# Optimization experiments

Hardware: AMD Instinct MI355X
Metric: run time of the kernel (lower is better)

Reference implementation:

```python
import jax, jax.numpy as jnp
import numpy as np

SEQ, BATCH, IN, HID, OUT = 512, 64, 512, 1024, 512
KEEP = 0.7  # dropout p = 0.3


def setup_inputs() -> dict:
    key = jax.random.key(0)
    ks = jax.random.split(key, 9)
    def lin(k, fan_out, fan_in):
        bound = 1.0 / np.sqrt(fan_in)
        kw, kb = jax.random.split(k)
        W = jax.random.uniform(kw, (fan_out, fan_in), jnp.float32, -bound, bound)
        b = jax.random.uniform(kb, (fan_out,), jnp.float32, -bound, bound)
        return W, b
    x = jax.random.normal(ks[0], (SEQ, BATCH, IN), jnp.float32)
    # inverted dropout mask, fixed for determinism
    drop_mask = (jax.random.bernoulli(ks[1], KEEP, (SEQ, BATCH, OUT))
                 .astype(jnp.float32) / KEEP)
    W_i2h, b_i2h = lin(ks[2], HID, IN + HID)
    W_i2o, b_i2o = lin(ks[3], OUT, IN + HID)
    W_o2o, b_o2o = lin(ks[4], OUT, HID + OUT)
    return {"x": x, "drop_mask": drop_mask,
            "W_i2h": W_i2h, "b_i2h": b_i2h,
            "W_i2o": W_i2o, "b_i2o": b_i2o,
            "W_o2o": W_o2o, "b_o2o": b_o2o}


def reference(x, drop_mask, W_i2h, b_i2h, W_i2o, b_i2o, W_o2o, b_o2o):
    # x: [S, B, IN]; returns log-probs [S, B, OUT]
    def step(h, inp):
        x_t, m_t = inp  # [B, IN], [B, OUT]
        comb = jnp.concatenate([x_t, h], axis=1)          # [B, IN+HID]
        out = comb @ W_i2o.T + b_i2o                      # [B, OUT]
        h_new = comb @ W_i2h.T + b_i2h                    # [B, HID]
        oc = jnp.concatenate([out, h_new], axis=1) @ W_o2o.T + b_o2o  # [B, OUT]
        oc = oc * m_t                                     # dropout (inverted mask)
        oc = jax.nn.log_softmax(oc, axis=-1)
        return h_new, oc
    h0 = jnp.zeros((x.shape[1], W_i2h.shape[0]), x.dtype)
    _, outs = jax.lax.scan(step, h0, (x, drop_mask))
    return outs
```

## Files before the change

kernel.cpp:

```cpp
#include <hip/hip_runtime.h>
#include <stdint.h>


typedef unsigned short ushort_t;
typedef __attribute__((ext_vector_type(8))) __bf16 bf16x8;
typedef __attribute__((ext_vector_type(4))) float f32x4;

__device__ __forceinline__ ushort_t f2bf(float f) {
  union { float f; uint32_t u; } v; v.f = f;
  uint32_t r = v.u + 0x7fffu + ((v.u >> 16) & 1u);
  return (ushort_t)(r >> 16);
}
__device__ __forceinline__ float bf2f(ushort_t b) {
  union { uint32_t u; float f; } v; v.u = ((uint32_t)b) << 16;
  return v.f;
}

__device__ __forceinline__ void gload16(const ushort_t* g, ushort_t* l) {
  __builtin_amdgcn_global_load_lds(
      (const __attribute__((address_space(1))) uint32_t*)g,
      (__attribute__((address_space(3))) uint32_t*)l, 16, 0, 0);
}

__global__ __launch_bounds__(256) void init_kernel(uint32_t* harr0) {
  int i = blockIdx.x * blockDim.x + threadIdx.x;
  if (i < 32768) harr0[i] = 0;
}

__global__ __launch_bounds__(256) void pack_kernel(
    const float* __restrict__ x, const float* __restrict__ W_i2h,
    const float* __restrict__ W_i2o, const float* __restrict__ W_o2o,
    ushort_t* xB, ushort_t* Wihx, ushort_t* Whh, ushort_t* Wiox,
    ushort_t* Wioh, ushort_t* Wo1, ushort_t* Wo2) {
  int64_t i = (int64_t)blockIdx.x * blockDim.x + threadIdx.x;
  const int64_t c0 = 16777216, c1 = 17301504, c2 = 18350080, c3 = 18612224,
                c4 = 19136512, c5 = 19398656, c6 = 19922944;
  if (i < c0) { xB[i] = f2bf(x[i]); return; }
  if (i < c1) { int64_t j = i - c0; int r = j >> 9,  c = j & 511;  Wihx[j] = f2bf(W_i2h[(int64_t)r * 1536 + c]); return; }
  if (i < c2) { int64_t j = i - c1; int r = j >> 10, c = j & 1023; Whh[j]  = f2bf(W_i2h[(int64_t)r * 1536 + 512 + c]); return; }
  if (i < c3) { int64_t j = i - c2; int r = j >> 9,  c = j & 511;  Wiox[j] = f2bf(W_i2o[(int64_t)r * 1536 + c]); return; }
  if (i < c4) { int64_t j = i - c3; int r = j >> 10, c = j & 1023; Wioh[j] = f2bf(W_i2o[(int64_t)r * 1536 + 512 + c]); return; }
  if (i < c5) { int64_t j = i - c4; int r = j >> 9,  c = j & 511;  Wo1[j]  = f2bf(W_o2o[(int64_t)r * 1536 + c]); return; }
  if (i < c6) { int64_t j = i - c5; int r = j >> 10, c = j & 1023; Wo2[j]  = f2bf(W_o2o[(int64_t)r * 1536 + 512 + c]); return; }
}

__global__ __launch_bounds__(256) void gemm_bt(
    const ushort_t* __restrict__ A1, int lda1, const ushort_t* __restrict__ B1, int K1,
    const ushort_t* __restrict__ A2, int lda2, const ushort_t* __restrict__ B2, int K2,
    const float* __restrict__ bias, float* Cf, ushort_t* Cb, int Ntiles) {
  __shared__ __align__(16) ushort_t AsF[4096];
  __shared__ __align__(16) ushort_t BsF[4096];
  const int mt = blockIdx.x & 255, nt = blockIdx.x >> 8;
  const int m0 = mt * 128, n0 = nt * 128;
  const int tid = threadIdx.x;
  const int w = tid >> 6, l = tid & 63;
  const int quad = l >> 4, l15 = l & 15;
  const int wm = (w & 1) * 64, wn = (w >> 1) * 64;
  const int r0 = tid >> 2, chunk = tid & 3;
  f32x4 acc[4][4] = {};

  for (int phase = 0; phase < 2; ++phase) {
    const ushort_t* A = phase ? A2 : A1;
    const ushort_t* B = phase ? B2 : B1;
    const int lda = phase ? lda2 : lda1;
    const int K = phase ? K2 : K1;
    for (int k0 = 0; k0 < K; k0 += 32) {
      __syncthreads();
      gload16(A + (size_t)(m0 + r0) * lda + k0 + chunk * 8,      &AsF[tid * 8]);
      gload16(A + (size_t)(m0 + r0 + 64) * lda + k0 + chunk * 8, &AsF[2048 + tid * 8]);
      gload16(B + (size_t)(n0 + r0) * K + k0 + chunk * 8,        &BsF[tid * 8]);
      gload16(B + (size_t)(n0 + r0 + 64) * K + k0 + chunk * 8,   &BsF[2048 + tid * 8]);
      __syncthreads();
      bf16x8 af[4], bfr[4];
#pragma unroll
      for (int i = 0; i < 4; ++i) af[i]  = *(const bf16x8*)&AsF[(wm + 16 * i + l15) * 32 + 8 * quad];
#pragma unroll
      for (int j = 0; j < 4; ++j) bfr[j] = *(const bf16x8*)&BsF[(wn + 16 * j + l15) * 32 + 8 * quad];
#pragma unroll
      for (int i = 0; i < 4; ++i)
#pragma unroll
        for (int j = 0; j < 4; ++j)
          acc[i][j] = __builtin_amdgcn_mfma_f32_16x16x32_bf16(af[i], bfr[j], acc[i][j], 0, 0, 0);
    }
  }

  const int N = Ntiles * 128;
#pragma unroll
  for (int i = 0; i < 4; ++i) {
    const int row = m0 + wm + 16 * i + 4 * quad;
#pragma unroll
    for (int j = 0; j < 4; ++j) {
      const int col = n0 + wn + 16 * j + l15;
      const float bv = bias[col];
#pragma unroll
      for (int r = 0; r < 4; ++r) {
        const float v = acc[i][j][r] + bv;
        const size_t idx = (size_t)(row + r) * N + col;
        if (Cf) Cf[idx] = v;
        else Cb[idx] = f2bf(v);
      }
    }
  }
}

__global__ __launch_bounds__(256) void gemm_bn(
    const ushort_t* __restrict__ Am, const ushort_t* __restrict__ Bm,
    ushort_t* __restrict__ Om) {
  __shared__ __align__(16) ushort_t AsF[4096];
  __shared__ __align__(16) ushort_t BsF[4096];
  const int mt = blockIdx.x >> 3, nt = blockIdx.x & 7;
  const int m0 = mt * 128, n0 = nt * 128;
  const int tid = threadIdx.x;
  const int w = tid >> 6, l = tid & 63;
  const int quad = l >> 4, l15 = l & 15;
  const int wm = (w & 1) * 64, wn = (w >> 1) * 64;
  const int r0 = tid >> 2, chunk = tid & 3;
  f32x4 acc[4][4] = {};
  for (int k0 = 0; k0 < 1024; k0 += 32) {
    __syncthreads();
    gload16(Am + (size_t)(m0 + r0) * 1024 + k0 + chunk * 8,      &AsF[tid * 8]);
    gload16(Am + (size_t)(m0 + r0 + 64) * 1024 + k0 + chunk * 8, &AsF[2048 + tid * 8]);
#pragma unroll
    for (int rep = 0; rep < 2; ++rep) {
      const int idx = tid + 256 * rep;
      const int kk = idx & 31, n8 = idx >> 5;
      union { uint4 v; ushort_t s[8]; } u;
      u.v = *(const uint4*)(Bm + (size_t)(k0 + kk) * 1024 + n0 + n8 * 8);
#pragma unroll
      for (int i = 0; i < 8; ++i) BsF[(n8 * 8 + i) * 32 + kk] = u.s[i];
    }
    __syncthreads();
    bf16x8 af[4], bfr[4];
#pragma unroll
    for (int i = 0; i < 4; ++i) af[i]  = *(const bf16x8*)&AsF[(wm + 16 * i + l15) * 32 + 8 * quad];
#pragma unroll
    for (int j = 0; j < 4; ++j) bfr[j] = *(const bf16x8*)&BsF[(wn + 16 * j + l15) * 32 + 8 * quad];
#pragma unroll
    for (int i = 0; i < 4; ++i)
#pragma unroll
      for (int j = 0; j < 4; ++j)
        acc[i][j] = __builtin_amdgcn_mfma_f32_16x16x32_bf16(af[i], bfr[j], acc[i][j], 0, 0, 0);
  }
#pragma unroll
  for (int i = 0; i < 4; ++i) {
    const int row = m0 + wm + 16 * i + 4 * quad;
#pragma unroll
    for (int j = 0; j < 4; ++j) {
      const int col = n0 + wn + 16 * j + l15;
#pragma unroll
      for (int r = 0; r < 4; ++r)
        Om[(size_t)(row + r) * 1024 + col] = f2bf(acc[i][j][r]);
    }
  }
}

__global__ __launch_bounds__(256) void rnn_step(
    const ushort_t* __restrict__ A, size_t aStride,
    const ushort_t* __restrict__ Xh, const ushort_t* __restrict__ Whh,
    ushort_t* __restrict__ O) {
  __shared__ __align__(16) ushort_t AsF[4096];
  __shared__ __align__(16) ushort_t BsF[4096];
  const int p = blockIdx.x >> 3;
  const int n0 = (blockIdx.x & 7) * 128;
  const int tid = threadIdx.x;
  const int w = tid >> 6, l = tid & 63;
  const int quad = l >> 4, l15 = l & 15;
  const int wm = (w & 1) * 64, wn = (w >> 1) * 64;
  const int r0 = tid >> 2, chunk = tid & 3;
  f32x4 acc[4][4] = {};
  const ushort_t* a0 = A + (size_t)(2 * p) * aStride + (size_t)r0 * 1024;
  const ushort_t* a1 = A + (size_t)(2 * p + 1) * aStride + (size_t)r0 * 1024;
  for (int k0 = 0; k0 < 1024; k0 += 32) {
    __syncthreads();
    gload16(a0 + k0 + chunk * 8, &AsF[tid * 8]);
    gload16(a1 + k0 + chunk * 8, &AsF[2048 + tid * 8]);
    gload16(Whh + (size_t)(n0 + r0) * 1024 + k0 + chunk * 8,      &BsF[tid * 8]);
    gload16(Whh + (size_t)(n0 + r0 + 64) * 1024 + k0 + chunk * 8, &BsF[2048 + tid * 8]);
    __syncthreads();
    bf16x8 af[4], bfr[4];
#pragma unroll
    for (int i = 0; i < 4; ++i) af[i]  = *(const bf16x8*)&AsF[(wm + 16 * i + l15) * 32 + 8 * quad];
#pragma unroll
    for (int j = 0; j < 4; ++j) bfr[j] = *(const bf16x8*)&BsF[(wn + 16 * j + l15) * 32 + 8 * quad];
#pragma unroll
    for (int i = 0; i < 4; ++i)
#pragma unroll
      for (int j = 0; j < 4; ++j)
        acc[i][j] = __builtin_amdgcn_mfma_f32_16x16x32_bf16(af[i], bfr[j], acc[i][j], 0, 0, 0);
  }
#pragma unroll
  for (int i = 0; i < 4; ++i) {
#pragma unroll
    for (int j = 0; j < 4; ++j) {
      const int col = n0 + wn + 16 * j + l15;
#pragma unroll
      for (int r = 0; r < 4; ++r) {
        const int gr = wm + 16 * i + 4 * quad + r;
        const int c = 2 * p + (gr >> 6);
        const size_t idx = (size_t)c * 524288 + (size_t)(gr & 63) * 1024 + col;
        O[idx] = f2bf(acc[i][j][r] + bf2f(Xh[idx]));
      }
    }
  }
}

__global__ __launch_bounds__(256) void scan_step(
    const ushort_t* __restrict__ Sold, const ushort_t* __restrict__ V,
    ushort_t* __restrict__ Snew, int d) {
  __shared__ __align__(16) ushort_t AsF[4096];
  __shared__ __align__(16) ushort_t BsF[4096];
  const int p = blockIdx.x >> 3;
  const int n0 = (blockIdx.x & 7) * 128;
  const int tid = threadIdx.x;
  const int w = tid >> 6, l = tid & 63;
  const int quad = l >> 4, l15 = l & 15;
  const int wm = (w & 1) * 64, wn = (w >> 1) * 64;
  const int r0 = tid >> 2, chunk = tid & 3;
  f32x4 acc[4][4] = {};
  const int j0 = 2 * p, j1 = 2 * p + 1;
  const int s0 = (j0 >= d) ? j0 - d : j0;
  const int s1 = (j1 >= d) ? j1 - d : j1;
  const ushort_t* a0 = Sold + (size_t)s0 * 65536 + (size_t)r0 * 1024;
  const ushort_t* a1 = Sold + (size_t)s1 * 65536 + (size_t)r0 * 1024;
  for (int k0 = 0; k0 < 1024; k0 += 32) {
    __syncthreads();
    gload16(a0 + k0 + chunk * 8, &AsF[tid * 8]);
    gload16(a1 + k0 + chunk * 8, &AsF[2048 + tid * 8]);
    gload16(V + (size_t)(n0 + r0) * 1024 + k0 + chunk * 8,      &BsF[tid * 8]);
    gload16(V + (size_t)(n0 + r0 + 64) * 1024 + k0 + chunk * 8, &BsF[2048 + tid * 8]);
    __syncthreads();
    bf16x8 af[4], bfr[4];
#pragma unroll
    for (int i = 0; i < 4; ++i) af[i]  = *(const bf16x8*)&AsF[(wm + 16 * i + l15) * 32 + 8 * quad];
#pragma unroll
    for (int j = 0; j < 4; ++j) bfr[j] = *(const bf16x8*)&BsF[(wn + 16 * j + l15) * 32 + 8 * quad];
#pragma unroll
    for (int i = 0; i < 4; ++i)
#pragma unroll
      for (int j = 0; j < 4; ++j)
        acc[i][j] = __builtin_amdgcn_mfma_f32_16x16x32_bf16(af[i], bfr[j], acc[i][j], 0, 0, 0);
  }
#pragma unroll
  for (int i = 0; i < 4; ++i) {
#pragma unroll
    for (int j = 0; j < 4; ++j) {
      const int col = n0 + wn + 16 * j + l15;
#pragma unroll
      for (int r = 0; r < 4; ++r) {
        const int gr = wm + 16 * i + 4 * quad + r;
        const int c = 2 * p + (gr >> 6);
        const size_t idx = (size_t)c * 65536 + (size_t)(gr & 63) * 1024 + col;
        const float g = (c >= d) ? acc[i][j][r] : 0.0f;
        Snew[idx] = f2bf(g + bf2f(Sold[idx]));
      }
    }
  }
}

__global__ __launch_bounds__(256) void correct_kernel(
    const ushort_t* __restrict__ S, ushort_t* __restrict__ Harr,
    const ushort_t* __restrict__ B1, const ushort_t* __restrict__ B2,
    const ushort_t* __restrict__ B3, const ushort_t* __restrict__ B4,
    const ushort_t* __restrict__ B5, const ushort_t* __restrict__ B6,
    const ushort_t* __restrict__ B7, const ushort_t* __restrict__ B8) {
  __shared__ __align__(16) ushort_t AsF[4096];
  __shared__ __align__(16) ushort_t BsF[4096];
  const int p = blockIdx.x >> 3;
  const int n0 = (blockIdx.x & 7) * 128;
  const int j = blockIdx.y + 1;
  const ushort_t* Wj;
  switch (j) {
    case 1: Wj = B1; break; case 2: Wj = B2; break;
    case 3: Wj = B3; break; case 4: Wj = B4; break;
    case 5: Wj = B5; break; case 6: Wj = B6; break;
    case 7: Wj = B7; break; default: Wj = B8; break;
  }
  ushort_t* XO = Harr + (size_t)j * 65536;
  const int tid = threadIdx.x;
  const int w = tid >> 6, l = tid & 63;
  const int quad = l >> 4, l15 = l & 15;
  const int wm = (w & 1) * 64, wn = (w >> 1) * 64;
  const int r0 = tid >> 2, chunk = tid & 3;
  f32x4 acc[4][4] = {};
  const ushort_t* a0 = S + (size_t)(2 * p) * 65536 + (size_t)r0 * 1024;
  const ushort_t* a1 = S + (size_t)(2 * p + 1) * 65536 + (size_t)r0 * 1024;
  for (int k0 = 0; k0 < 1024; k0 += 32) {
    __syncthreads();
    gload16(a0 + k0 + chunk * 8, &AsF[tid * 8]);
    gload16(a1 + k0 + chunk * 8, &AsF[2048 + tid * 8]);
    gload16(Wj + (size_t)(n0 + r0) * 1024 + k0 + chunk * 8,      &BsF[tid * 8]);
    gload16(Wj + (size_t)(n0 + r0 + 64) * 1024 + k0 + chunk * 8, &BsF[2048 + tid * 8]);
    __syncthreads();
    bf16x8 af[4], bfr[4];
#pragma unroll
    for (int i = 0; i < 4; ++i) af[i]  = *(const bf16x8*)&AsF[(wm + 16 * i + l15) * 32 + 8 * quad];
#pragma unroll
    for (int jj = 0; jj < 4; ++jj) bfr[jj] = *(const bf16x8*)&BsF[(wn + 16 * jj + l15) * 32 + 8 * quad];
#pragma unroll
    for (int i = 0; i < 4; ++i)
#pragma unroll
      for (int jj = 0; jj < 4; ++jj)
        acc[i][jj] = __builtin_amdgcn_mfma_f32_16x16x32_bf16(af[i], bfr[jj], acc[i][jj], 0, 0, 0);
  }
#pragma unroll
  for (int i = 0; i < 4; ++i) {
#pragma unroll
    for (int jj = 0; jj < 4; ++jj) {
      const int col = n0 + wn + 16 * jj + l15;
#pragma unroll
      for (int r = 0; r < 4; ++r) {
        const int gr = wm + 16 * i + 4 * quad + r;
        const int c = 2 * p + (gr >> 6);
        const size_t idx = (size_t)c * 524288 + (size_t)(gr & 63) * 1024 + col;
        XO[idx] = f2bf(acc[i][jj][r] + bf2f(XO[idx]));
      }
    }
  }
}

__global__ __launch_bounds__(256) void copy_strided(
    ushort_t* __restrict__ dst, size_t dStride,
    const ushort_t* __restrict__ src, size_t sStride) {
  const int c = blockIdx.x >> 5, part = blockIdx.x & 31;
  const size_t off = (size_t)part * 2048 + (size_t)threadIdx.x * 8;
  *(uint4*)(dst + (size_t)c * dStride + off) = *(const uint4*)(src + (size_t)c * sStride + off);
}

__global__ __launch_bounds__(256) void softmax_kernel(
    float* __restrict__ out, const float* __restrict__ mask) {
  const int row = blockIdx.x;
  const int tid = threadIdx.x;
  const size_t base = (size_t)row * 512;
  __shared__ float sm[4], ss[4];
  const float v0 = out[base + tid] * mask[base + tid];
  const float v1 = out[base + tid + 256] * mask[base + tid + 256];
  float m = fmaxf(v0, v1);
#pragma unroll
  for (int off = 32; off; off >>= 1) m = fmaxf(m, __shfl_xor(m, off, 64));
  const int w = tid >> 6;
  if ((tid & 63) == 0) sm[w] = m;
  __syncthreads();
  m = fmaxf(fmaxf(sm[0], sm[1]), fmaxf(sm[2], sm[3]));
  float s = __expf(v0 - m) + __expf(v1 - m);
#pragma unroll
  for (int off = 32; off; off >>= 1) s += __shfl_xor(s, off, 64);
  if ((tid & 63) == 0) ss[w] = s;
  __syncthreads();
  s = ss[0] + ss[1] + ss[2] + ss[3];
  const float lg = logf(s);
  out[base + tid] = v0 - m - lg;
  out[base + tid + 256] = v1 - m - lg;
}

extern "C" void kernel_launch(void* const* d_in, const int* in_sizes, int n_in,
                              void* d_out, int out_size, void* d_ws, size_t ws_size,
                              hipStream_t stream) {
  const float* x     = (const float*)d_in[0];
  const float* mask  = (const float*)d_in[1];
  const float* W_i2h = (const float*)d_in[2];
  const float* b_i2h = (const float*)d_in[3];
  const float* W_i2o = (const float*)d_in[4];
  const float* b_i2o = (const float*)d_in[5];
  const float* W_o2o = (const float*)d_in[6];
  const float* b_o2o = (const float*)d_in[7];
  float* out = (float*)d_out;

  char* ws = (char*)d_ws;
  const size_t NEED = 207753216;
  if (ws_size < NEED) return;
  ushort_t* xB   = (ushort_t*)(ws + 0);
  ushort_t* XhB  = (ushort_t*)(ws + 33554432);
  ushort_t* Harr = (ushort_t*)(ws + 100663296);
  char* outbRegion = ws + 167903232;
  ushort_t* OUTB = (ushort_t*)outbRegion;
  ushort_t* SA = (ushort_t*)(outbRegion + 0);
  ushort_t* SB = (ushort_t*)(outbRegion + 8388608);
  ushort_t* PB = (ushort_t*)(outbRegion + 16777216);
  ushort_t* P2 = PB, *P4 = PB + 1048576, *P8 = PB + 2097152,
          * S3 = PB + 3145728, *S5 = PB + 4194304, *S6 = PB + 5242880,
          * S7 = PB + 6291456, *P256 = PB + 7340032;
  ushort_t* P16 = S3, *P32 = S5, *P64 = S6, *P128 = S7;
  ushort_t* Wihx = (ushort_t*)(ws + 201457664);
  ushort_t* Whh  = (ushort_t*)(ws + 202506240);
  ushort_t* Wiox = (ushort_t*)(ws + 204603392);
  ushort_t* Wioh = (ushort_t*)(ws + 205127680);
  ushort_t* Wo1  = (ushort_t*)(ws + 206176256);
  ushort_t* Wo2  = (ushort_t*)(ws + 206700544);

  hipLaunchKernelGGL(init_kernel, dim3(128), dim3(256), 0, stream, (uint32_t*)Harr);
  hipLaunchKernelGGL(pack_kernel, dim3(77824), dim3(256), 0, stream,
                     x, W_i2h, W_i2o, W_o2o, xB, Wihx, Whh, Wiox, Wioh, Wo1, Wo2);
  hipLaunchKernelGGL(gemm_bt, dim3(2048), dim3(256), 0, stream,
                     xB, 512, Wihx, 512, (const ushort_t*)nullptr, 0,
                     (const ushort_t*)nullptr, 0, b_i2h, (float*)nullptr, XhB, 8);
  hipLaunchKernelGGL(gemm_bn, dim3(64), dim3(256), 0, stream, Whh, Whh, P2);
  hipLaunchKernelGGL(gemm_bn, dim3(64), dim3(256), 0, stream, P2, P2, P4);
  hipLaunchKernelGGL(gemm_bn, dim3(64), dim3(256), 0, stream, P4, P4, P8);
  hipLaunchKernelGGL(gemm_bn, dim3(64), dim3(256), 0, stream, P8, P8, P16);
  hipLaunchKernelGGL(gemm_bn, dim3(64), dim3(256), 0, stream, P16, P16, P32);
  hipLaunchKernelGGL(gemm_bn, dim3(64), dim3(256), 0, stream, P32, P32, P64);
  hipLaunchKernelGGL(gemm_bn, dim3(64), dim3(256), 0, stream, P64, P64, P128);
  hipLaunchKernelGGL(gemm_bn, dim3(64), dim3(256), 0, stream, P128, P128, P256);
  hipLaunchKernelGGL(copy_strided, dim3(2048), dim3(256), 0, stream,
                     Harr + 65536, (size_t)524288, XhB, (size_t)524288);
  for (int k = 1; k < 8; ++k)
    hipLaunchKernelGGL(rnn_step, dim3(256), dim3(256), 0, stream,
                       Harr + (size_t)k * 65536, (size_t)524288,
                       XhB + (size_t)k * 65536, Whh, Harr + (size_t)(k + 1) * 65536);
  hipLaunchKernelGGL(copy_strided, dim3(2048), dim3(256), 0, stream,
                     SA, (size_t)65536, Harr, (size_t)524288);
  hipLaunchKernelGGL(scan_step, dim3(256), dim3(256), 0, stream, SA, P8,   SB, 1);
  hipLaunchKernelGGL(scan_step, dim3(256), dim3(256), 0, stream, SB, P16,  SA, 2);
  hipLaunchKernelGGL(scan_step, dim3(256), dim3(256), 0, stream, SA, P32,  SB, 4);
  hipLaunchKernelGGL(scan_step, dim3(256), dim3(256), 0, stream, SB, P64,  SA, 8);
  hipLaunchKernelGGL(scan_step, dim3(256), dim3(256), 0, stream, SA, P128, SB, 16);
  hipLaunchKernelGGL(scan_step, dim3(256), dim3(256), 0, stream, SB, P256, SA, 32);
  hipLaunchKernelGGL(gemm_bn, dim3(64), dim3(256), 0, stream, Whh, P2, S3);
  hipLaunchKernelGGL(gemm_bn, dim3(64), dim3(256), 0, stream, Whh, P4, S5);
  hipLaunchKernelGGL(gemm_bn, dim3(64), dim3(256), 0, stream, P2,  P4, S6);
  hipLaunchKernelGGL(gemm_bn, dim3(64), dim3(256), 0, stream, S3,  P4, S7);
  hipLaunchKernelGGL(correct_kernel, dim3(256, 8), dim3(256), 0, stream,
                     SA, Harr, Whh, P2, S3, P4, S5, S6, S7, P8);
  hipLaunchKernelGGL(gemm_bt, dim3(1024), dim3(256), 0, stream,
                     xB, 512, Wiox, 512, Harr, 1024, Wioh, 1024,
                     b_i2o, (float*)nullptr, OUTB, 4);
  hipLaunchKernelGGL(gemm_bt, dim3(1024), dim3(256), 0, stream,
                     OUTB, 512, Wo1, 512, Harr + 65536, 1024, Wo2, 1024,
                     b_o2o, out, (ushort_t*)nullptr, 4);
  hipLaunchKernelGGL(softmax_kernel, dim3(32768), dim3(256), 0, stream, out, mask);
}
```

Before: 1.254 ms.

## Fuse scan phases into persistent kernel and fold output projections algebraically

Replaces the many separate rnn_step, scan_step and power-matrix gemm launches with one persistent kernel of 256 blocks that uses a global atomic-counter barrier between stages. It also overlaps the power-matrix products with the recurrent steps. The output path is re-associated algebraically: W_o2o's first half is premultiplied into W_i2o (U1, U2) and a combined bias, so one fused GEMM with three K phases produces the logits directly, and the mask multiply moves into its epilogue. This removes launch overhead and the intermediate OUTB round trip. The costs are spin-wait grid barriers that assume all 256 blocks are co-resident, and a different bf16 rounding order in the folded weights.

```diff
diff --git a/kernel.cpp b/kernel.cpp
--- a/kernel.cpp
+++ b/kernel.cpp
@@ -15,26 +15,27 @@
   union { uint32_t u; float f; } v; v.u = ((uint32_t)b) << 16;
   return v.f;
 }
-
 __device__ __forceinline__ void gload16(const ushort_t* g, ushort_t* l) {
   __builtin_amdgcn_global_load_lds(
       (const __attribute__((address_space(1))) uint32_t*)g,
       (__attribute__((address_space(3))) uint32_t*)l, 16, 0, 0);
 }
 
-__global__ __launch_bounds__(256) void init_kernel(uint32_t* harr0) {
+__global__ __launch_bounds__(256) void init_kernel(uint32_t* harr0, int* cnt) {
   int i = blockIdx.x * blockDim.x + threadIdx.x;
   if (i < 32768) harr0[i] = 0;
+  if (i < 16) cnt[i] = 0;
 }
 
 __global__ __launch_bounds__(256) void pack_kernel(
     const float* __restrict__ x, const float* __restrict__ W_i2h,
     const float* __restrict__ W_i2o, const float* __restrict__ W_o2o,
+    const float* __restrict__ b_i2o, const float* __restrict__ b_o2o,
     ushort_t* xB, ushort_t* Wihx, ushort_t* Whh, ushort_t* Wiox,
-    ushort_t* Wioh, ushort_t* Wo1, ushort_t* Wo2) {
+    ushort_t* Wioh, ushort_t* Wo1, ushort_t* Wo2, float* biasP) {
   int64_t i = (int64_t)blockIdx.x * blockDim.x + threadIdx.x;
   const int64_t c0 = 16777216, c1 = 17301504, c2 = 18350080, c3 = 18612224,
-                c4 = 19136512, c5 = 19398656, c6 = 19922944;
+                c4 = 19136512, c5 = 19398656, c6 = 19922944, c7 = 19923456;
   if (i < c0) { xB[i] = f2bf(x[i]); return; }
   if (i < c1) { int64_t j = i - c0; int r = j >> 9,  c = j & 511;  Wihx[j] = f2bf(W_i2h[(int64_t)r * 1536 + c]); return; }
   if (i < c2) { int64_t j = i - c1; int r = j >> 10, c = j & 1023; Whh[j]  = f2bf(W_i2h[(int64_t)r * 1536 + 512 + c]); return; }
@@ -42,12 +43,18 @@
   if (i < c4) { int64_t j = i - c3; int r = j >> 10, c = j & 1023; Wioh[j] = f2bf(W_i2o[(int64_t)r * 1536 + 512 + c]); return; }
   if (i < c5) { int64_t j = i - c4; int r = j >> 9,  c = j & 511;  Wo1[j]  = f2bf(W_o2o[(int64_t)r * 1536 + c]); return; }
   if (i < c6) { int64_t j = i - c5; int r = j >> 10, c = j & 1023; Wo2[j]  = f2bf(W_o2o[(int64_t)r * 1536 + 512 + c]); return; }
+  if (i < c7) {
+    int n = (int)(i - c6);
+    const float* wr = W_o2o + (int64_t)n * 1536;
+    float s = 0.f;
+    for (int m = 0; m < 512; ++m) s += wr[m] * b_i2o[m];
+    biasP[n] = s + b_o2o[n];
+  }
 }
 
 __global__ __launch_bounds__(256) void gemm_bt(
     const ushort_t* __restrict__ A1, int lda1, const ushort_t* __restrict__ B1, int K1,
-    const ushort_t* __restrict__ A2, int lda2, const ushort_t* __restrict__ B2, int K2,
-    const float* __restrict__ bias, float* Cf, ushort_t* Cb, int Ntiles) {
+    const float* __restrict__ bias, ushort_t* Cb, int Ntiles) {
   __shared__ __align__(16) ushort_t AsF[4096];
   __shared__ __align__(16) ushort_t BsF[4096];
   const int mt = blockIdx.x & 255, nt = blockIdx.x >> 8;
@@ -58,32 +65,24 @@
   const int wm = (w & 1) * 64, wn = (w >> 1) * 64;
   const int r0 = tid >> 2, chunk = tid & 3;
   f32x4 acc[4][4] = {};
-
-  for (int phase = 0; phase < 2; ++phase) {
-    const ushort_t* A = phase ? A2 : A1;
-    const ushort_t* B = phase ? B2 : B1;
-    const int lda = phase ? lda2 : lda1;
-    const int K = phase ? K2 : K1;
-    for (int k0 = 0; k0 < K; k0 += 32) {
-      __syncthreads();
-      gload16(A + (size_t)(m0 + r0) * lda + k0 + chunk * 8,      &AsF[tid * 8]);
-      gload16(A + (size_t)(m0 + r0 + 64) * lda + k0 + chunk * 8, &AsF[2048 + tid * 8]);
-      gload16(B + (size_t)(n0 + r0) * K + k0 + chunk * 8,        &BsF[tid * 8]);
-      gload16(B + (size_t)(n0 + r0 + 64) * K + k0 + chunk * 8,   &BsF[2048 + tid * 8]);
-      __syncthreads();
-      bf16x8 af[4], bfr[4];
-#pragma unroll
-      for (int i = 0; i < 4; ++i) af[i]  = *(const bf16x8*)&AsF[(wm + 16 * i + l15) * 32 + 8 * quad];
-#pragma unroll
-      for (int j = 0; j < 4; ++j) bfr[j] = *(const bf16x8*)&BsF[(wn + 16 * j + l15) * 32 + 8 * quad];
-#pragma unroll
-      for (int i = 0; i < 4; ++i)
-#pragma unroll
-        for (int j = 0; j < 4; ++j)
-          acc[i][j] = __builtin_amdgcn_mfma_f32_16x16x32_bf16(af[i], bfr[j], acc[i][j], 0, 0, 0);
-    }
-  }
-
+  for (int k0 = 0; k0 < K1; k0 += 32) {
+    __syncthreads();
+    gload16(A1 + (size_t)(m0 + r0) * lda1 + k0 + chunk * 8,      &AsF[tid * 8]);
+    gload16(A1 + (size_t)(m0 + r0 + 64) * lda1 + k0 + chunk * 8, &AsF[2048 + tid * 8]);
+    gload16(B1 + (size_t)(n0 + r0) * K1 + k0 + chunk * 8,        &BsF[tid * 8]);
+    gload16(B1 + (size_t)(n0 + r0 + 64) * K1 + k0 + chunk * 8,   &BsF[2048 + tid * 8]);
+    __syncthreads();
+    bf16x8 af[4], bfr[4];
+#pragma unroll
+    for (int i = 0; i < 4; ++i) af[i]  = *(const bf16x8*)&AsF[(wm + 16 * i + l15) * 32 + 8 * quad];
+#pragma unroll
+    for (int j = 0; j < 4; ++j) bfr[j] = *(const bf16x8*)&BsF[(wn + 16 * j + l15) * 32 + 8 * quad];
+#pragma unroll
+    for (int i = 0; i < 4; ++i)
+#pragma unroll
+      for (int j = 0; j < 4; ++j)
+        acc[i][j] = __builtin_amdgcn_mfma_f32_16x16x32_bf16(af[i], bfr[j], acc[i][j], 0, 0, 0);
+  }
   const int N = Ntiles * 128;
 #pragma unroll
   for (int i = 0; i < 4; ++i) {
@@ -93,23 +92,74 @@
       const int col = n0 + wn + 16 * j + l15;
       const float bv = bias[col];
 #pragma unroll
-      for (int r = 0; r < 4; ++r) {
-        const float v = acc[i][j][r] + bv;
-        const size_t idx = (size_t)(row + r) * N + col;
-        if (Cf) Cf[idx] = v;
-        else Cb[idx] = f2bf(v);
-      }
-    }
-  }
-}
-
-__global__ __launch_bounds__(256) void gemm_bn(
-    const ushort_t* __restrict__ Am, const ushort_t* __restrict__ Bm,
-    ushort_t* __restrict__ Om) {
+      for (int r = 0; r < 4; ++r)
+        Cb[(size_t)(row + r) * N + col] = f2bf(acc[i][j][r] + bv);
+    }
+  }
+}
+
+__global__ __launch_bounds__(256) void usetup_kernel(
+    const ushort_t* __restrict__ Wo1, const ushort_t* __restrict__ Wiox,
+    const ushort_t* __restrict__ Wioh, ushort_t* __restrict__ U1,
+    ushort_t* __restrict__ U2) {
   __shared__ __align__(16) ushort_t AsF[4096];
   __shared__ __align__(16) ushort_t BsF[4096];
-  const int mt = blockIdx.x >> 3, nt = blockIdx.x & 7;
+  int job = blockIdx.x;
+  const ushort_t* Bm; ushort_t* Om; int mt, nt, ldb;
+  if (job < 16) { mt = job >> 2; nt = job & 3; Bm = Wiox; Om = U1; ldb = 512; }
+  else { job -= 16; mt = job >> 3; nt = job & 7; Bm = Wioh; Om = U2; ldb = 1024; }
   const int m0 = mt * 128, n0 = nt * 128;
+  const int tid = threadIdx.x;
+  const int w = tid >> 6, l = tid & 63;
+  const int quad = l >> 4, l15 = l & 15;
+  const int wm = (w & 1) * 64, wn = (w >> 1) * 64;
+  const int r0 = tid >> 2, chunk = tid & 3;
+  f32x4 acc[4][4] = {};
+  for (int k0 = 0; k0 < 512; k0 += 32) {
+    __syncthreads();
+    gload16(Wo1 + (size_t)(m0 + r0) * 512 + k0 + chunk * 8,      &AsF[tid * 8]);
+    gload16(Wo1 + (size_t)(m0 + r0 + 64) * 512 + k0 + chunk * 8, &AsF[2048 + tid * 8]);
+#pragma unroll
+    for (int rep = 0; rep < 2; ++rep) {
+      const int idx = tid + 256 * rep;
+      const int kk = idx & 31, n8 = idx >> 5;
+      union { uint4 v; ushort_t s[8]; } u;
+      u.v = *(const uint4*)(Bm + (size_t)(k0 + kk) * ldb + n0 + n8 * 8);
+#pragma unroll
+      for (int i = 0; i < 8; ++i) BsF[(n8 * 8 + i) * 32 + kk] = u.s[i];
+    }
+    __syncthreads();
+    bf16x8 af[4], bfr[4];
+#pragma unroll
+    for (int i = 0; i < 4; ++i) af[i]  = *(const bf16x8*)&AsF[(wm + 16 * i + l15) * 32 + 8 * quad];
+#pragma unroll
+    for (int j = 0; j < 4; ++j) bfr[j] = *(const bf16x8*)&BsF[(wn + 16 * j + l15) * 32 + 8 * quad];
+#pragma unroll
+    for (int i = 0; i < 4; ++i)
+#pragma unroll
+      for (int j = 0; j < 4; ++j)
+        acc[i][j] = __builtin_amdgcn_mfma_f32_16x16x32_bf16(af[i], bfr[j], acc[i][j], 0, 0, 0);
+  }
+#pragma unroll
+  for (int i = 0; i < 4; ++i) {
+    const int row = m0 + wm + 16 * i + 4 * quad;
+#pragma unroll
+    for (int j = 0; j < 4; ++j) {
+      const int col = n0 + wn + 16 * j + l15;
+#pragma unroll
+      for (int r = 0; r < 4; ++r)
+        Om[(size_t)(row + r) * ldb + col] = f2bf(acc[i][j][r]);
+    }
+  }
+}
+
+__device__ void tile_job(
+    const ushort_t* a0, const ushort_t* a1,
+    const ushort_t* B, int btr, int n0,
+    const ushort_t* x0, const ushort_t* x1,
+    ushort_t* o0, ushort_t* o1, int g0, int g1) {
+  __shared__ __align__(16) ushort_t AsF[4096];
+  __shared__ __align__(16) ushort_t BsF[4096];
   const int tid = threadIdx.x;
   const int w = tid >> 6, l = tid & 63;
   const int quad = l >> 4, l15 = l & 15;
@@ -118,16 +168,21 @@
   f32x4 acc[4][4] = {};
   for (int k0 = 0; k0 < 1024; k0 += 32) {
     __syncthreads();
-    gload16(Am + (size_t)(m0 + r0) * 1024 + k0 + chunk * 8,      &AsF[tid * 8]);
-    gload16(Am + (size_t)(m0 + r0 + 64) * 1024 + k0 + chunk * 8, &AsF[2048 + tid * 8]);
-#pragma unroll
-    for (int rep = 0; rep < 2; ++rep) {
-      const int idx = tid + 256 * rep;
-      const int kk = idx & 31, n8 = idx >> 5;
-      union { uint4 v; ushort_t s[8]; } u;
-      u.v = *(const uint4*)(Bm + (size_t)(k0 + kk) * 1024 + n0 + n8 * 8);
-#pragma unroll
-      for (int i = 0; i < 8; ++i) BsF[(n8 * 8 + i) * 32 + kk] = u.s[i];
+    gload16(a0 + (size_t)r0 * 1024 + k0 + chunk * 8, &AsF[tid * 8]);
+    gload16(a1 + (size_t)r0 * 1024 + k0 + chunk * 8, &AsF[2048 + tid * 8]);
+    if (!btr) {
+      gload16(B + (size_t)(n0 + r0) * 1024 + k0 + chunk * 8,      &BsF[tid * 8]);
+      gload16(B + (size_t)(n0 + r0 + 64) * 1024 + k0 + chunk * 8, &BsF[2048 + tid * 8]);
+    } else {
+#pragma unroll
+      for (int rep = 0; rep < 2; ++rep) {
+        const int idx = tid + 256 * rep;
+        const int kk = idx & 31, n8 = idx >> 5;
+        union { uint4 v; ushort_t s[8]; } u;
+        u.v = *(const uint4*)(B + (size_t)(k0 + kk) * 1024 + n0 + n8 * 8);
+#pragma unroll
+        for (int i = 0; i < 8; ++i) BsF[(n8 * 8 + i) * 32 + kk] = u.s[i];
+      }
     }
     __syncthreads();
     bf16x8 af[4], bfr[4];
@@ -143,117 +198,106 @@
   }
 #pragma unroll
   for (int i = 0; i < 4; ++i) {
-    const int row = m0 + wm + 16 * i + 4 * quad;
 #pragma unroll
     for (int j = 0; j < 4; ++j) {
       const int col = n0 + wn + 16 * j + l15;
 #pragma unroll
-      for (int r = 0; r < 4; ++r)
-        Om[(size_t)(row + r) * 1024 + col] = f2bf(acc[i][j][r]);
-    }
-  }
-}
-
-__global__ __launch_bounds__(256) void rnn_step(
-    const ushort_t* __restrict__ A, size_t aStride,
-    const ushort_t* __restrict__ Xh, const ushort_t* __restrict__ Whh,
-    ushort_t* __restrict__ O) {
-  __shared__ __align__(16) ushort_t AsF[4096];
-  __shared__ __align__(16) ushort_t BsF[4096];
-  const int p = blockIdx.x >> 3;
-  const int n0 = (blockIdx.x & 7) * 128;
-  const int tid = threadIdx.x;
-  const int w = tid >> 6, l = tid & 63;
-  const int quad = l >> 4, l15 = l & 15;
-  const int wm = (w & 1) * 64, wn = (w >> 1) * 64;
-  const int r0 = tid >> 2, chunk = tid & 3;
-  f32x4 acc[4][4] = {};
-  const ushort_t* a0 = A + (size_t)(2 * p) * aStride + (size_t)r0 * 1024;
-  const ushort_t* a1 = A + (size_t)(2 * p + 1) * aStride + (size_t)r0 * 1024;
-  for (int k0 = 0; k0 < 1024; k0 += 32) {
-    __syncthreads();
-    gload16(a0 + k0 + chunk * 8, &AsF[tid * 8]);
-    gload16(a1 + k0 + chunk * 8, &AsF[2048 + tid * 8]);
-    gload16(Whh + (size_t)(n0 + r0) * 1024 + k0 + chunk * 8,      &BsF[tid * 8]);
-    gload16(Whh + (size_t)(n0 + r0 + 64) * 1024 + k0 + chunk * 8, &BsF[2048 + tid * 8]);
-    __syncthreads();
-    bf16x8 af[4], bfr[4];
-#pragma unroll
-    for (int i = 0; i < 4; ++i) af[i]  = *(const bf16x8*)&AsF[(wm + 16 * i + l15) * 32 + 8 * quad];
-#pragma unroll
-    for (int j = 0; j < 4; ++j) bfr[j] = *(const bf16x8*)&BsF[(wn + 16 * j + l15) * 32 + 8 * quad];
-#pragma unroll
-    for (int i = 0; i < 4; ++i)
-#pragma unroll
-      for (int j = 0; j < 4; ++j)
-        acc[i][j] = __builtin_amdgcn_mfma_f32_16x16x32_bf16(af[i], bfr[j], acc[i][j], 0, 0, 0);
-  }
-#pragma unroll
-  for (int i = 0; i < 4; ++i) {
-#pragma unroll
-    for (int j = 0; j < 4; ++j) {
-      const int col = n0 + wn + 16 * j + l15;
-#pragma unroll
       for (int r = 0; r < 4; ++r) {
         const int gr = wm + 16 * i + 4 * quad + r;
-        const int c = 2 * p + (gr >> 6);
-        const size_t idx = (size_t)c * 524288 + (size_t)(gr & 63) * 1024 + col;
-        O[idx] = f2bf(acc[i][j][r] + bf2f(Xh[idx]));
-      }
-    }
-  }
-}
-
-__global__ __launch_bounds__(256) void scan_step(
-    const ushort_t* __restrict__ Sold, const ushort_t* __restrict__ V,
-    ushort_t* __restrict__ Snew, int d) {
-  __shared__ __align__(16) ushort_t AsF[4096];
-  __shared__ __align__(16) ushort_t BsF[4096];
-  const int p = blockIdx.x >> 3;
-  const int n0 = (blockIdx.x & 7) * 128;
-  const int tid = threadIdx.x;
-  const int w = tid >> 6, l = tid & 63;
-  const int quad = l >> 4, l15 = l & 15;
-  const int wm = (w & 1) * 64, wn = (w >> 1) * 64;
-  const int r0 = tid >> 2, chunk = tid & 3;
-  f32x4 acc[4][4] = {};
-  const int j0 = 2 * p, j1 = 2 * p + 1;
-  const int s0 = (j0 >= d) ? j0 - d : j0;
-  const int s1 = (j1 >= d) ? j1 - d : j1;
-  const ushort_t* a0 = Sold + (size_t)s0 * 65536 + (size_t)r0 * 1024;
-  const ushort_t* a1 = Sold + (size_t)s1 * 65536 + (size_t)r0 * 1024;
-  for (int k0 = 0; k0 < 1024; k0 += 32) {
-    __syncthreads();
-    gload16(a0 + k0 + chunk * 8, &AsF[tid * 8]);
-    gload16(a1 + k0 + chunk * 8, &AsF[2048 + tid * 8]);
-    gload16(V + (size_t)(n0 + r0) * 1024 + k0 + chunk * 8,      &BsF[tid * 8]);
-    gload16(V + (size_t)(n0 + r0 + 64) * 1024 + k0 + chunk * 8, &BsF[2048 + tid * 8]);
-    __syncthreads();
-    bf16x8 af[4], bfr[4];
-#pragma unroll
-    for (int i = 0; i < 4; ++i) af[i]  = *(const bf16x8*)&AsF[(wm + 16 * i + l15) * 32 + 8 * quad];
-#pragma unroll
-    for (int j = 0; j < 4; ++j) bfr[j] = *(const bf16x8*)&BsF[(wn + 16 * j + l15) * 32 + 8 * quad];
-#pragma unroll
-    for (int i = 0; i < 4; ++i)
-#pragma unroll
-      for (int j = 0; j < 4; ++j)
-        acc[i][j] = __builtin_amdgcn_mfma_f32_16x16x32_bf16(af[i], bfr[j], acc[i][j], 0, 0, 0);
-  }
-#pragma unroll
-  for (int i = 0; i < 4; ++i) {
-#pragma unroll
-    for (int j = 0; j < 4; ++j) {
-      const int col = n0 + wn + 16 * j + l15;
-#pragma unroll
-      for (int r = 0; r < 4; ++r) {
-        const int gr = wm + 16 * i + 4 * quad + r;
-        const int c = 2 * p + (gr >> 6);
-        const size_t idx = (size_t)c * 65536 + (size_t)(gr & 63) * 1024 + col;
-        const float g = (c >= d) ? acc[i][j][r] : 0.0f;
-        Snew[idx] = f2bf(g + bf2f(Sold[idx]));
-      }
-    }
+        const int half = gr >> 6, rr = gr & 63;
+        float v = (half ? g1 : g0) ? acc[i][j][r] : 0.0f;
+        const ushort_t* xx = half ? x1 : x0;
+        if (xx) v += bf2f(xx[(size_t)rr * 1024 + col]);
+        (half ? o1 : o0)[(size_t)rr * 1024 + col] = f2bf(v);
+      }
+    }
+  }
+}
+
+__device__ __forceinline__ void gsync(int* cnt, int s) {
+  __threadfence();
+  __syncthreads();
+  if (threadIdx.x == 0) {
+    atomicAdd(&cnt[s], 1);
+    while (__hip_atomic_load(&cnt[s], __ATOMIC_RELAXED, __HIP_MEMORY_SCOPE_AGENT) < 256) {}
+  }
+  __syncthreads();
+  __threadfence();
+}
+
+#define PWp(idx) (Pw + (size_t)(idx) * 1048576)
+
+__global__ __launch_bounds__(256) void scan_mega(
+    const ushort_t* __restrict__ XhB, ushort_t* __restrict__ Harr,
+    ushort_t* __restrict__ Pw, ushort_t* __restrict__ SA,
+    ushort_t* __restrict__ SB, const ushort_t* __restrict__ Whh,
+    int* __restrict__ cnt) {
+  const int bid = blockIdx.x;
+  const int tid = threadIdx.x;
+
+  if (bid < 64) {
+    const ushort_t* src = XhB + (size_t)bid * 524288;
+    ushort_t* dst = Harr + 65536 + (size_t)bid * 524288;
+#pragma unroll
+    for (int it = 0; it < 32; ++it)
+      *(uint4*)(dst + it * 2048 + tid * 8) = *(const uint4*)(src + it * 2048 + tid * 8);
+  } else if (bid < 128) {
+    const int t = bid - 64, mt = t >> 3, nt = t & 7;
+    const ushort_t* a0 = Whh + (size_t)mt * 131072;
+    tile_job(a0, a0 + 65536, Whh, 1, nt * 128, nullptr, nullptr,
+             PWp(0) + (size_t)mt * 131072, PWp(0) + (size_t)mt * 131072 + 65536, 1, 1);
+  }
+  gsync(cnt, 0);
+
+  for (int k = 1; k <= 7; ++k) {
+    {
+      const int p = bid & 31, nt = bid >> 5;
+      const size_t c0 = (size_t)(2 * p) * 524288, c1 = c0 + 524288;
+      tile_job(Harr + (size_t)k * 65536 + c0, Harr + (size_t)k * 65536 + c1,
+               Whh, 0, nt * 128,
+               XhB + (size_t)k * 65536 + c0, XhB + (size_t)k * 65536 + c1,
+               Harr + (size_t)(k + 1) * 65536 + c0,
+               Harr + (size_t)(k + 1) * 65536 + c1, 1, 1);
+    }
+    {
+      const ushort_t *A = nullptr, *Bp = nullptr; ushort_t* O = nullptr;
+      const int pj = bid >> 6, t = bid & 63;
+      if (k == 1) {
+        if (pj == 0)      { A = Whh;    Bp = PWp(0); O = PWp(1); }
+        else if (pj == 1) { A = PWp(0); Bp = PWp(0); O = PWp(2); }
+      } else if (k == 2) {
+        if (pj == 0)      { A = Whh;    Bp = PWp(2); O = PWp(3); }
+        else if (pj == 1) { A = PWp(0); Bp = PWp(2); O = PWp(4); }
+        else if (pj == 2) { A = PWp(1); Bp = PWp(2); O = PWp(5); }
+        else              { A = PWp(2); Bp = PWp(2); O = PWp(6); }
+      } else if (pj == 0) {
+        A = PWp(3 + k); Bp = A; O = PWp(4 + k);
+      }
+      if (A) {
+        const int mt = t >> 3, nt2 = t & 7;
+        tile_job(A + (size_t)mt * 131072, A + (size_t)mt * 131072 + 65536,
+                 Bp, 1, nt2 * 128, nullptr, nullptr,
+                 O + (size_t)mt * 131072, O + (size_t)mt * 131072 + 65536, 1, 1);
+      }
+    }
+    gsync(cnt, k);
+  }
+
+  for (int si = 0; si < 6; ++si) {
+    const int d = 1 << si;
+    const ushort_t* oldB; size_t oldStr; ushort_t* nw;
+    if (si == 0)      { oldB = Harr; oldStr = 524288; nw = SB; }
+    else if (si & 1)  { oldB = SB;   oldStr = 65536;  nw = SA; }
+    else              { oldB = SA;   oldStr = 65536;  nw = SB; }
+    const int p = bid & 31, nt = bid >> 5;
+    const int ca = 2 * p, cb = ca + 1;
+    const int ia = ca >= d ? ca - d : ca, ib = cb >= d ? cb - d : cb;
+    tile_job(oldB + (size_t)ia * oldStr, oldB + (size_t)ib * oldStr,
+             PWp(6 + si), 0, nt * 128,
+             oldB + (size_t)ca * oldStr, oldB + (size_t)cb * oldStr,
+             nw + (size_t)ca * 65536, nw + (size_t)cb * 65536,
+             ca >= d, cb >= d);
+    if (si < 5) gsync(cnt, 8 + si);
   }
 }
 
@@ -318,22 +362,67 @@
   }
 }
 
-__global__ __launch_bounds__(256) void copy_strided(
-    ushort_t* __restrict__ dst, size_t dStride,
-    const ushort_t* __restrict__ src, size_t sStride) {
-  const int c = blockIdx.x >> 5, part = blockIdx.x & 31;
-  const size_t off = (size_t)part * 2048 + (size_t)threadIdx.x * 8;
-  *(uint4*)(dst + (size_t)c * dStride + off) = *(const uint4*)(src + (size_t)c * sStride + off);
-}
-
-__global__ __launch_bounds__(256) void softmax_kernel(
-    float* __restrict__ out, const float* __restrict__ mask) {
+__global__ __launch_bounds__(256) void gemm_fused(
+    const ushort_t* __restrict__ xB, const ushort_t* __restrict__ U1,
+    const ushort_t* __restrict__ Harr, const ushort_t* __restrict__ U2,
+    const ushort_t* __restrict__ Wo2, const float* __restrict__ biasP,
+    const float* __restrict__ mask, float* __restrict__ out) {
+  __shared__ __align__(16) ushort_t AsF[4096];
+  __shared__ __align__(16) ushort_t BsF[4096];
+  const int mt = blockIdx.x & 255, nt = blockIdx.x >> 8;
+  const int m0 = mt * 128, n0 = nt * 128;
+  const int tid = threadIdx.x;
+  const int w = tid >> 6, l = tid & 63;
+  const int quad = l >> 4, l15 = l & 15;
+  const int wm = (w & 1) * 64, wn = (w >> 1) * 64;
+  const int r0 = tid >> 2, chunk = tid & 3;
+  f32x4 acc[4][4] = {};
+  for (int ph = 0; ph < 3; ++ph) {
+    const ushort_t* A = ph == 0 ? xB : (ph == 1 ? Harr : Harr + 65536);
+    const ushort_t* B = ph == 0 ? U1 : (ph == 1 ? U2 : Wo2);
+    const int K = ph == 0 ? 512 : 1024;
+    for (int k0 = 0; k0 < K; k0 += 32) {
+      __syncthreads();
+      gload16(A + (size_t)(m0 + r0) * K + k0 + chunk * 8,      &AsF[tid * 8]);
+      gload16(A + (size_t)(m0 + r0 + 64) * K + k0 + chunk * 8, &AsF[2048 + tid * 8]);
+      gload16(B + (size_t)(n0 + r0) * K + k0 + chunk * 8,      &BsF[tid * 8]);
+      gload16(B + (size_t)(n0 + r0 + 64) * K + k0 + chunk * 8, &BsF[2048 + tid * 8]);
+      __syncthreads();
+      bf16x8 af[4], bfr[4];
+#pragma unroll
+      for (int i = 0; i < 4; ++i) af[i]  = *(const bf16x8*)&AsF[(wm + 16 * i + l15) * 32 + 8 * quad];
+#pragma unroll
+      for (int j = 0; j < 4; ++j) bfr[j] = *(const bf16x8*)&BsF[(wn + 16 * j + l15) * 32 + 8 * quad];
+#pragma unroll
+      for (int i = 0; i < 4; ++i)
+#pragma unroll
+        for (int j = 0; j < 4; ++j)
+          acc[i][j] = __builtin_amdgcn_mfma_f32_16x16x32_bf16(af[i], bfr[j], acc[i][j], 0, 0, 0);
+    }
+  }
+#pragma unroll
+  for (int i = 0; i < 4; ++i) {
+    const int row = m0 + wm + 16 * i + 4 * quad;
+#pragma unroll
+    for (int j = 0; j < 4; ++j) {
+      const int col = n0 + wn + 16 * j + l15;
+      const float bv = biasP[col];
+#pragma unroll
+      for (int r = 0; r < 4; ++r) {
+        const size_t idx = (size_t)(row + r) * 512 + col;
+        out[idx] = (acc[i][j][r] + bv) * mask[idx];
+      }
+    }
+  }
+}
+
+__global__ __launch_bounds__(256) void softmax_kernel(float* __restrict__ out) {
   const int row = blockIdx.x;
   const int tid = threadIdx.x;
   const size_t base = (size_t)row * 512;
   __shared__ float sm[4], ss[4];
-  const float v0 = out[base + tid] * mask[base + tid];
-  const float v1 = out[base + tid + 256] * mask[base + tid + 256];
+  const float v0 = out[base + tid];
+  const float v1 = out[base + tid + 256];
   float m = fmaxf(v0, v1);
 #pragma unroll
   for (int off = 32; off; off >>= 1) m = fmaxf(m, __shfl_xor(m, off, 64));
@@ -370,62 +459,37 @@
   if (ws_size < NEED) return;
   ushort_t* xB   = (ushort_t*)(ws + 0);
   ushort_t* XhB  = (ushort_t*)(ws + 33554432);
+  ushort_t* SA   = (ushort_t*)(ws + 33554432);
+  ushort_t* SB   = (ushort_t*)(ws + 41943040);
   ushort_t* Harr = (ushort_t*)(ws + 100663296);
-  char* outbRegion = ws + 167903232;
-  ushort_t* OUTB = (ushort_t*)outbRegion;
-  ushort_t* SA = (ushort_t*)(outbRegion + 0);
-  ushort_t* SB = (ushort_t*)(outbRegion + 8388608);
-  ushort_t* PB = (ushort_t*)(outbRegion + 16777216);
-  ushort_t* P2 = PB, *P4 = PB + 1048576, *P8 = PB + 2097152,
-          * S3 = PB + 3145728, *S5 = PB + 4194304, *S6 = PB + 5242880,
-          * S7 = PB + 6291456, *P256 = PB + 7340032;
-  ushort_t* P16 = S3, *P32 = S5, *P64 = S6, *P128 = S7;
+  ushort_t* Pw   = (ushort_t*)(ws + 167903232);
+  ushort_t* U1   = (ushort_t*)(ws + 193069056);
+  ushort_t* U2   = (ushort_t*)(ws + 193593344);
+  float* biasP   = (float*)(ws + 194641920);
   ushort_t* Wihx = (ushort_t*)(ws + 201457664);
   ushort_t* Whh  = (ushort_t*)(ws + 202506240);
   ushort_t* Wiox = (ushort_t*)(ws + 204603392);
   ushort_t* Wioh = (ushort_t*)(ws + 205127680);
   ushort_t* Wo1  = (ushort_t*)(ws + 206176256);
   ushort_t* Wo2  = (ushort_t*)(ws + 206700544);
-
-  hipLaunchKernelGGL(init_kernel, dim3(128), dim3(256), 0, stream, (uint32_t*)Harr);
-  hipLaunchKernelGGL(pack_kernel, dim3(77824), dim3(256), 0, stream,
-                     x, W_i2h, W_i2o, W_o2o, xB, Wihx, Whh, Wiox, Wioh, Wo1, Wo2);
+  int* cnt       = (int*)(ws + 207749120);
+
+  hipLaunchKernelGGL(init_kernel, dim3(128), dim3(256), 0, stream,
+                     (uint32_t*)Harr, cnt);
+  hipLaunchKernelGGL(pack_kernel, dim3(77826), dim3(256), 0, stream,
+                     x, W_i2h, W_i2o, W_o2o, b_i2o, b_o2o,
+                     xB, Wihx, Whh, Wiox, Wioh, Wo1, Wo2, biasP);
   hipLaunchKernelGGL(gemm_bt, dim3(2048), dim3(256), 0, stream,
-                     xB, 512, Wihx, 512, (const ushort_t*)nullptr, 0,
-                     (const ushort_t*)nullptr, 0, b_i2h, (float*)nullptr, XhB, 8);
-  hipLaunchKernelGGL(gemm_bn, dim3(64), dim3(256), 0, stream, Whh, Whh, P2);
-  hipLaunchKernelGGL(gemm_bn, dim3(64), dim3(256), 0, stream, P2, P2, P4);
-  hipLaunchKernelGGL(gemm_bn, dim3(64), dim3(256), 0, stream, P4, P4, P8);
-  hipLaunchKernelGGL(gemm_bn, dim3(64), dim3(256), 0, stream, P8, P8, P16);
-  hipLaunchKernelGGL(gemm_bn, dim3(64), dim3(256), 0, stream, P16, P16, P32);
-  hipLaunchKernelGGL(gemm_bn, dim3(64), dim3(256), 0, stream, P32, P32, P64);
-  hipLaunchKernelGGL(gemm_bn, dim3(64), dim3(256), 0, stream, P64, P64, P128);
-  hipLaunchKernelGGL(gemm_bn, dim3(64), dim3(256), 0, stream, P128, P128, P256);
-  hipLaunchKernelGGL(copy_strided, dim3(2048), dim3(256), 0, stream,
-                     Harr + 65536, (size_t)524288, XhB, (size_t)524288);
-  for (int k = 1; k < 8; ++k)
-    hipLaunchKernelGGL(rnn_step, dim3(256), dim3(256), 0, stream,
-                       Harr + (size_t)k * 65536, (size_t)524288,
-                       XhB + (size_t)k * 65536, Whh, Harr + (size_t)(k + 1) * 65536);
-  hipLaunchKernelGGL(copy_strided, dim3(2048), dim3(256), 0, stream,
-                     SA, (size_t)65536, Harr, (size_t)524288);
-  hipLaunchKernelGGL(scan_step, dim3(256), dim3(256), 0, stream, SA, P8,   SB, 1);
-  hipLaunchKernelGGL(scan_step, dim3(256), dim3(256), 0, stream, SB, P16,  SA, 2);
-  hipLaunchKernelGGL(scan_step, dim3(256), dim3(256), 0, stream, SA, P32,  SB, 4);
-  hipLaunchKernelGGL(scan_step, dim3(256), dim3(256), 0, stream, SB, P64,  SA, 8);
-  hipLaunchKernelGGL(scan_step, dim3(256), dim3(256), 0, stream, SA, P128, SB, 16);
-  hipLaunchKernelGGL(scan_step, dim3(256), dim3(256), 0, stream, SB, P256, SA, 32);
-  hipLaunchKernelGGL(gemm_bn, dim3(64), dim3(256), 0, stream, Whh, P2, S3);
-  hipLaunchKernelGGL(gemm_bn, dim3(64), dim3(256), 0, stream, Whh, P4, S5);
-  hipLaunchKernelGGL(gemm_bn, dim3(64), dim3(256), 0, stream, P2,  P4, S6);
-  hipLaunchKernelGGL(gemm_bn, dim3(64), dim3(256), 0, stream, S3,  P4, S7);
-  hipLaunchKernelGGL(correct_kernel, dim3(256, 8), dim3(256), 0, stream,
-                     SA, Harr, Whh, P2, S3, P4, S5, S6, S7, P8);
-  hipLaunchKernelGGL(gemm_bt, dim3(1024), dim3(256), 0, stream,
-                     xB, 512, Wiox, 512, Harr, 1024, Wioh, 1024,
-                     b_i2o, (float*)nullptr, OUTB, 4);
-  hipLaunchKernelGGL(gemm_bt, dim3(1024), dim3(256), 0, stream,
-                     OUTB, 512, Wo1, 512, Harr + 65536, 1024, Wo2, 1024,
-                     b_o2o, out, (ushort_t*)nullptr, 4);
-  hipLaunchKernelGGL(softmax_kernel, dim3(32768), dim3(256), 0, stream, out, mask);
-}
+                     xB, 512, Wihx, 512, b_i2h, XhB, 8);
+  hipLaunchKernelGGL(usetup_kernel, dim3(48), dim3(256), 0, stream,
+                     Wo1, Wiox, Wioh, U1, U2);
+  hipLaunchKernelGGL(scan_mega, dim3(256), dim3(256), 0, stream,
+                     XhB, Harr, Pw, SA, SB, Whh, cnt);
+  hipLaunchKernelGGL(correct_kernel, dim3(dim3(256, 8)), dim3(256), 0, stream,
+                     SA, Harr,
+                     Whh, Pw, Pw + 1048576, Pw + 2097152, Pw + 3145728,
+                     Pw + 4194304, Pw + 5242880, Pw + 6291456);
+  hipLaunchKernelGGL(gemm_fused, dim3(1024), dim3(256), 0, stream,
+                     xB, U1, Harr, U2, Wo2, biasP, mask, out);
+  hipLaunchKernelGGL(softmax_kernel, dim3(32768), dim3(256), 0, stream, out);
+}
```

New measurement: 1.926 ms. +53.6%, slower.
